# Kernel tuning notes

Hardware: AMD Instinct MI355X
Metric: run time of the kernel (lower is better)

Reference implementation:

```python
import jax, jax.numpy as jnp
import numpy as np

B = 1024      # batch
E = 1024      # encoding_dim
OUT = 34      # 17 joints x 2 coords


def setup_inputs() -> dict:
    key = jax.random.key(0)
    ks = jax.random.split(key, 8)
    s = 0.02  # weight init scale
    return {
        "h": jax.random.normal(ks[0], (B, E), dtype=jnp.float32),
        "c": jax.random.normal(ks[1], (B, E), dtype=jnp.float32),
        "W_ih": jax.random.normal(ks[2], (4 * E, E), dtype=jnp.float32) * s,
        "W_hh": jax.random.normal(ks[3], (4 * E, E), dtype=jnp.float32) * s,
        "b_ih": jax.random.normal(ks[4], (4 * E,), dtype=jnp.float32) * s,
        "b_hh": jax.random.normal(ks[5], (4 * E,), dtype=jnp.float32) * s,
        "W_out": jax.random.normal(ks[6], (OUT, E), dtype=jnp.float32) * s,
        "b_out": jax.random.normal(ks[7], (OUT,), dtype=jnp.float32) * s,
        "future_preds": 10,
    }


def reference(h, c, W_ih, W_hh, b_ih, b_hh, W_out, b_out, future_preds):
    E_ = h.shape[1]
    start = jnp.zeros_like(h)  # zeros=True start token

    def step(carry, _):
        h_t, c_t, x = carry
        # LSTMCell: gates in PyTorch order i, f, g, o
        gates = x @ W_ih.T + b_ih + h_t @ W_hh.T + b_hh  # [B, 4E]
        i = jax.nn.sigmoid(gates[:, 0 * E_:1 * E_])
        f = jax.nn.sigmoid(gates[:, 1 * E_:2 * E_])
        g = jnp.tanh(gates[:, 2 * E_:3 * E_])
        o = jax.nn.sigmoid(gates[:, 3 * E_:4 * E_])
        c_new = f * c_t + i * g
        h_new = o * jnp.tanh(c_new)
        return (h_new, c_new, h_new), h_new

    _, hs = jax.lax.scan(step, (h, c, start), None, length=future_preds)
    # hs: [T, B, E] -> [B, T, E]
    preds = jnp.transpose(hs, (1, 0, 2))
    return preds @ W_out.T + b_out  # [B, T, 34]
```

## Files before the change

kernel.cpp:

```cpp
#include <hip/hip_runtime.h>
#include <cstdint>
#include <cstddef>

#define E_DIM   1024
#define B_DIM   1024
#define T_STEPS 10
#define OUT_DIM 34
#define OUT_PAD 48
#define HSTR    24
#define QK      256
#define WQ_ELEMS (64 * QK)
#define DYN_LDS (2 * WQ_ELEMS * 2 + 128 * HSTR * 2)

typedef __attribute__((ext_vector_type(4))) float  f32x4;
typedef __attribute__((ext_vector_type(8))) __bf16 bf16x8;

__device__ __forceinline__ unsigned short f2bf(float f) {
    unsigned int u = __float_as_uint(f);
    u = (u + 0x7FFFu + ((u >> 16) & 1u)) >> 16;
    return (unsigned short)u;
}
__device__ __forceinline__ float sigmoid_(float x) { return 1.0f / (1.0f + __expf(-x)); }
__device__ __forceinline__ float tanh_(float x)    { return 2.0f / (1.0f + __expf(-2.0f * x)) - 1.0f; }

__global__ void prep_weights(const float* __restrict__ W_ih, const float* __restrict__ W_hh,
                             const float* __restrict__ b_ih, const float* __restrict__ b_hh,
                             unsigned short* __restrict__ Wsum, unsigned short* __restrict__ Whh,
                             float* __restrict__ bperm) {
    const int n = blockIdx.x;
    const int g = (n >> 4) & 3;
    const int e = ((n >> 6) << 4) | (n & 15);
    const int srow = g * E_DIM + e;
    const size_t src = (size_t)srow * E_DIM;
    const int k = threadIdx.x * 4;
    float4 wi = *(const float4*)(W_ih + src + k);
    float4 wh = *(const float4*)(W_hh + src + k);
    const size_t dst = (size_t)n * E_DIM + k;
    Wsum[dst + 0] = f2bf(wi.x + wh.x);
    Wsum[dst + 1] = f2bf(wi.y + wh.y);
    Wsum[dst + 2] = f2bf(wi.z + wh.z);
    Wsum[dst + 3] = f2bf(wi.w + wh.w);
    Whh[dst + 0] = f2bf(wh.x);
    Whh[dst + 1] = f2bf(wh.y);
    Whh[dst + 2] = f2bf(wh.z);
    Whh[dst + 3] = f2bf(wh.w);
    if (threadIdx.x == 0) bperm[n] = b_ih[srow] + b_hh[srow];
}

__global__ void prep_state(const float* __restrict__ h0, const float* __restrict__ W_out,
                           unsigned short* __restrict__ hbuf, unsigned short* __restrict__ Woutp) {
    const int b = blockIdx.x;
    const int t = threadIdx.x;
    if (b < 1024) {
        const size_t i = ((size_t)b * 256 + t) * 4;
        float4 hv = *(const float4*)(h0 + i);
        hbuf[i + 0] = f2bf(hv.x);
        hbuf[i + 1] = f2bf(hv.y);
        hbuf[i + 2] = f2bf(hv.z);
        hbuf[i + 3] = f2bf(hv.w);
    } else {
        const int o = b - 1024;
        const int k = t * 4;
        float4 w = make_float4(0.f, 0.f, 0.f, 0.f);
        if (o < OUT_DIM) w = *(const float4*)(W_out + (size_t)o * E_DIM + k);
        const size_t dst = (size_t)o * E_DIM + k;
        Woutp[dst + 0] = f2bf(w.x);
        Woutp[dst + 1] = f2bf(w.y);
        Woutp[dst + 2] = f2bf(w.z);
        Woutp[dst + 3] = f2bf(w.w);
    }
}

__global__ void prep_c(const float* __restrict__ c0, float* __restrict__ C) {
    const int m = blockIdx.x;
    const int e0 = threadIdx.x * 4;
    float4 v = *(const float4*)(c0 + (size_t)m * E_DIM + e0);
    const int bm = m >> 7, wave = (m >> 5) & 3, mt = (m >> 4) & 1, q = (m >> 2) & 3, r = m & 3;
    const float vv[4] = {v.x, v.y, v.z, v.w};
#pragma unroll
    for (int ii = 0; ii < 4; ++ii) {
        const int e = e0 + ii;
        const int bn = e >> 4, j = e & 15;
        const int lane = q * 16 + j;
        C[(((size_t)(bn * 8 + bm) * 4 + wave) * 64 + lane) * 8 + mt * 4 + r] = vv[ii];
    }
}

__global__ __launch_bounds__(256, 2) void lstm_step(
    const unsigned short* __restrict__ Wp,
    const float* __restrict__ bp,
    const unsigned short* __restrict__ Hin,
    float* __restrict__ C,
    unsigned short* __restrict__ Hout)
{
    extern __shared__ __align__(16) unsigned short smem[];
    unsigned short* Wbuf0 = smem;
    unsigned short* Wbuf1 = smem + WQ_ELEMS;
    unsigned short* Ht    = smem + 2 * WQ_ELEMS;

    const int tid  = threadIdx.x;
    const int wave = tid >> 6;
    const int lane = tid & 63;
    const int bn = blockIdx.x;
    const int bm = blockIdx.y;
    const int j  = lane & 15;
    const int q  = lane >> 4;
    const int j7 = j & 7;

    f32x4 acc[2][4];
#pragma unroll
    for (int a = 0; a < 2; ++a)
#pragma unroll
        for (int b = 0; b < 4; ++b) acc[a][b] = (f32x4){0.f, 0.f, 0.f, 0.f};

    const int nb = bn * 64 + j;
    const float bi = bp[nb +  0];
    const float bf = bp[nb + 16];
    const float bg = bp[nb + 32];
    const float bo = bp[nb + 48];
    const size_t cbase = (((size_t)(bn * 8 + bm) * 4 + wave) * 64 + lane) * 8;
    float4 cold0 = *(const float4*)(C + cbase);
    float4 cold1 = *(const float4*)(C + cbase + 4);

    const unsigned short* arow0 = Hin + (size_t)(bm * 128 + wave * 32 + j) * E_DIM + q * 8;
    const unsigned short* arow1 = arow0 + (size_t)16 * E_DIM;
    const unsigned short* wrow  = Wp + (size_t)(bn * 64) * E_DIM;

    uint4 ra[8][2];
#pragma unroll
    for (int p = 0; p < 8; ++p) {
        ra[p][0] = *(const uint4*)(arow0 + p * 32);
        ra[p][1] = *(const uint4*)(arow1 + p * 32);
    }

    uint4 wreg[8];
#pragma unroll
    for (int i = 0; i < 8; ++i) {
        const int s = i * 256 + tid, row = s >> 5, c = s & 31;
        wreg[i] = *(const uint4*)(wrow + (size_t)row * E_DIM + c * 8);
    }
#pragma unroll
    for (int i = 0; i < 8; ++i) {
        const int s = i * 256 + tid, row = s >> 5, c = s & 31;
        *(uint4*)(Wbuf0 + row * QK + ((c ^ (row & 7)) << 3)) = wreg[i];
    }
    __syncthreads();

    for (int qtr = 0; qtr < 4; ++qtr) {
        if (qtr < 3) {
#pragma unroll
            for (int i = 0; i < 8; ++i) {
                const int s = i * 256 + tid, row = s >> 5, c = s & 31;
                wreg[i] = *(const uint4*)(wrow + (size_t)row * E_DIM + (qtr + 1) * QK + c * 8);
            }
        }
        const unsigned short* wb = (qtr & 1) ? Wbuf1 : Wbuf0;
#pragma unroll
        for (int ks8 = 0; ks8 < 8; ++ks8) {
            const int ks = qtr * 8 + ks8;
            bf16x8 av0 = __builtin_bit_cast(bf16x8, ra[ks & 7][0]);
            bf16x8 av1 = __builtin_bit_cast(bf16x8, ra[ks & 7][1]);
            const int coff = ((ks8 * 4 + q) ^ j7) << 3;
            bf16x8 bv[4];
#pragma unroll
            for (int nt = 0; nt < 4; ++nt)
                bv[nt] = *(const bf16x8*)(wb + (nt * 16 + j) * QK + coff);
#pragma unroll
            for (int nt = 0; nt < 4; ++nt) {
                acc[0][nt] = __builtin_amdgcn_mfma_f32_16x16x32_bf16(av0, bv[nt], acc[0][nt], 0, 0, 0);
                acc[1][nt] = __builtin_amdgcn_mfma_f32_16x16x32_bf16(av1, bv[nt], acc[1][nt], 0, 0, 0);
            }
            if (ks < 24) {
                ra[ks & 7][0] = *(const uint4*)(arow0 + (ks + 8) * 32);
                ra[ks & 7][1] = *(const uint4*)(arow1 + (ks + 8) * 32);
            }
        }
        if (qtr < 3) {
            unsigned short* wn_ = ((qtr + 1) & 1) ? Wbuf1 : Wbuf0;
#pragma unroll
            for (int i = 0; i < 8; ++i) {
                const int s = i * 256 + tid, row = s >> 5, c = s & 31;
                *(uint4*)(wn_ + row * QK + ((c ^ (row & 7)) << 3)) = wreg[i];
            }
            __syncthreads();
        }
    }

    float4 cnew[2];
    const float coldv[2][4] = {{cold0.x, cold0.y, cold0.z, cold0.w},
                               {cold1.x, cold1.y, cold1.z, cold1.w}};
#pragma unroll
    for (int mt = 0; mt < 2; ++mt) {
#pragma unroll
        for (int r = 0; r < 4; ++r) {
            const float iv = sigmoid_(acc[mt][0][r] + bi);
            const float fv = sigmoid_(acc[mt][1][r] + bf);
            const float gv = tanh_(acc[mt][2][r] + bg);
            const float ov = sigmoid_(acc[mt][3][r] + bo);
            const float cn = fv * coldv[mt][r] + iv * gv;
            cnew[mt][r] = cn;
            const int rowl = wave * 32 + mt * 16 + q * 4 + r;
            Ht[rowl * HSTR + j] = f2bf(ov * tanh_(cn));
        }
    }
    *(float4*)(C + cbase)     = cnew[0];
    *(float4*)(C + cbase + 4) = cnew[1];
    __syncthreads();

    {
        const int row = tid >> 1, part = tid & 1;
        uint4 v = *(const uint4*)(Ht + row * HSTR + part * 8);
        *(uint4*)(Hout + (size_t)(bm * 128 + row) * E_DIM + bn * 16 + part * 8) = v;
    }
}

__global__ __launch_bounds__(256) void proj_kernel(
    const unsigned short* __restrict__ Hs,
    const unsigned short* __restrict__ Wo,
    const float* __restrict__ b_out,
    float* __restrict__ Out)
{
    __shared__ float red[4][32][OUT_PAD];

    const int tid = threadIdx.x, wave = tid >> 6, lane = tid & 63;
    const int j = lane & 15, q = lane >> 4;
    const int t  = blockIdx.y;
    const int bb = blockIdx.x;
    const unsigned short* Hbase = Hs + ((size_t)t * B_DIM + (size_t)bb * 32) * E_DIM;
    const int k0 = wave * 256;

    f32x4 acc[2][3];
#pragma unroll
    for (int a = 0; a < 2; ++a)
#pragma unroll
        for (int b = 0; b < 3; ++b) acc[a][b] = (f32x4){0.f, 0.f, 0.f, 0.f};

#pragma unroll
    for (int kk = 0; kk < 256; kk += 32) {
        const int kc = k0 + kk + q * 8;
        bf16x8 av[2], bv[3];
#pragma unroll
        for (int mt = 0; mt < 2; ++mt)
            av[mt] = *(const bf16x8*)(Hbase + (size_t)(mt * 16 + j) * E_DIM + kc);
#pragma unroll
        for (int nt = 0; nt < 3; ++nt)
            bv[nt] = *(const bf16x8*)(Wo + (size_t)(nt * 16 + j) * E_DIM + kc);
#pragma unroll
        for (int mt = 0; mt < 2; ++mt)
#pragma unroll
            for (int nt = 0; nt < 3; ++nt)
                acc[mt][nt] = __builtin_amdgcn_mfma_f32_16x16x32_bf16(av[mt], bv[nt], acc[mt][nt], 0, 0, 0);
    }

#pragma unroll
    for (int mt = 0; mt < 2; ++mt)
#pragma unroll
        for (int nt = 0; nt < 3; ++nt)
#pragma unroll
            for (int r = 0; r < 4; ++r)
                red[wave][mt * 16 + q * 4 + r][nt * 16 + j] = acc[mt][nt][r];
    __syncthreads();

#pragma unroll
    for (int ii = 0; ii < 6; ++ii) {
        const int idx = tid * 6 + ii;
        const int row = idx / OUT_PAD, o = idx % OUT_PAD;
        if (o < OUT_DIM) {
            const float s = red[0][row][o] + red[1][row][o] + red[2][row][o] + red[3][row][o];
            Out[((size_t)(bb * 32 + row) * T_STEPS + t) * OUT_DIM + o] = s + b_out[o];
        }
    }
}

extern "C" void kernel_launch(void* const* d_in, const int* in_sizes, int n_in,
                              void* d_out, int out_size, void* d_ws, size_t ws_size,
                              hipStream_t stream) {
    (void)in_sizes; (void)n_in; (void)out_size; (void)ws_size;
    const float* h     = (const float*)d_in[0];
    const float* c     = (const float*)d_in[1];
    const float* W_ih  = (const float*)d_in[2];
    const float* W_hh  = (const float*)d_in[3];
    const float* b_ih  = (const float*)d_in[4];
    const float* b_hh  = (const float*)d_in[5];
    const float* W_out = (const float*)d_in[6];
    const float* b_out = (const float*)d_in[7];
    float* out = (float*)d_out;

    char* ws = (char*)d_ws;
    unsigned short* Wsum  = (unsigned short*)(ws + 0);
    unsigned short* Whh   = (unsigned short*)(ws + 8388608);
    float*          bperm = (float*)(ws + 16777216);
    unsigned short* Woutp = (unsigned short*)(ws + 16842752);
    float*          cbuf  = (float*)(ws + 16941056);
    unsigned short* hs    = (unsigned short*)(ws + 21135360);

    hipFuncSetAttribute((const void*)lstm_step,
                        hipFuncAttributeMaxDynamicSharedMemorySize, DYN_LDS);

    prep_weights<<<4096, 256, 0, stream>>>(W_ih, W_hh, b_ih, b_hh, Wsum, Whh, bperm);
    prep_state<<<1072, 256, 0, stream>>>(h, W_out, hs, Woutp);
    prep_c<<<1024, 256, 0, stream>>>(c, cbuf);

    lstm_step<<<dim3(64, 8), 256, DYN_LDS, stream>>>(Whh, bperm, hs, cbuf,
                                                     hs + (size_t)B_DIM * E_DIM);
    for (int t = 1; t < T_STEPS; ++t)
        lstm_step<<<dim3(64, 8), 256, DYN_LDS, stream>>>(Wsum, bperm,
                                                         hs + (size_t)t * B_DIM * E_DIM,
                                                         cbuf,
                                                         hs + (size_t)(t + 1) * B_DIM * E_DIM);

    proj_kernel<<<dim3(32, T_STEPS), 256, 0, stream>>>(hs + (size_t)B_DIM * E_DIM,
                                                       Woutp, b_out, out);
}
```

Before: 333.3 us.

## Pre-arrange LSTM weights in MFMA fragment order for contiguous loads

The weight prep kernel now writes W_ih+W_hh and W_hh in bf16, pre-permuted into the exact per-lane MFMA B-fragment order for each block's tile and K quarter. The step kernel can then stream each quarter with fully contiguous global loads and read LDS at lane*8 strides, with no XOR swizzle or row/column index math. The bias permutation moves into prep_state, and prep_weights launches far fewer, larger blocks. In exchange the prep kernel issues scattered 2-byte stores, and the LDS read pattern loses the swizzle that was there to avoid bank conflicts.

```diff
diff --git a/kernel.cpp b/kernel.cpp
--- a/kernel.cpp
+++ b/kernel.cpp
@@ -23,32 +23,37 @@
 __device__ __forceinline__ float sigmoid_(float x) { return 1.0f / (1.0f + __expf(-x)); }
 __device__ __forceinline__ float tanh_(float x)    { return 2.0f / (1.0f + __expf(-2.0f * x)) - 1.0f; }
 
-__global__ void prep_weights(const float* __restrict__ W_ih, const float* __restrict__ W_hh,
-                             const float* __restrict__ b_ih, const float* __restrict__ b_hh,
-                             unsigned short* __restrict__ Wsum, unsigned short* __restrict__ Whh,
-                             float* __restrict__ bperm) {
-    const int n = blockIdx.x;
-    const int g = (n >> 4) & 3;
-    const int e = ((n >> 6) << 4) | (n & 15);
-    const int srow = g * E_DIM + e;
-    const size_t src = (size_t)srow * E_DIM;
-    const int k = threadIdx.x * 4;
-    float4 wi = *(const float4*)(W_ih + src + k);
-    float4 wh = *(const float4*)(W_hh + src + k);
-    const size_t dst = (size_t)n * E_DIM + k;
-    Wsum[dst + 0] = f2bf(wi.x + wh.x);
-    Wsum[dst + 1] = f2bf(wi.y + wh.y);
-    Wsum[dst + 2] = f2bf(wi.z + wh.z);
-    Wsum[dst + 3] = f2bf(wi.w + wh.w);
-    Whh[dst + 0] = f2bf(wh.x);
-    Whh[dst + 1] = f2bf(wh.y);
-    Whh[dst + 2] = f2bf(wh.z);
-    Whh[dst + 3] = f2bf(wh.w);
-    if (threadIdx.x == 0) bperm[n] = b_ih[srow] + b_hh[srow];
+__global__ void prep_weights_frag(const float* __restrict__ W_ih, const float* __restrict__ W_hh,
+                                  unsigned short* __restrict__ WsumF, unsigned short* __restrict__ WhhF) {
+    const int bn = blockIdx.x >> 2, qtr = blockIdx.x & 3;
+    const int nt = threadIdx.x >> 6, lane = threadIdx.x & 63;
+    const int j = lane & 15, q = lane >> 4;
+    const int srow = nt * E_DIM + bn * 16 + j;
+    const float* wi = W_ih + (size_t)srow * E_DIM;
+    const float* wh = W_hh + (size_t)srow * E_DIM;
+    const size_t dstb = (size_t)bn * 65536 + (size_t)qtr * 16384 + nt * 512 + lane * 8;
+#pragma unroll
+    for (int ks8 = 0; ks8 < 8; ++ks8) {
+        const int k = qtr * 256 + ks8 * 32 + q * 8;
+        float4 i0 = *(const float4*)(wi + k);
+        float4 i1 = *(const float4*)(wi + k + 4);
+        float4 h0 = *(const float4*)(wh + k);
+        float4 h1 = *(const float4*)(wh + k + 4);
+        unsigned short* ds = WsumF + dstb + ks8 * 2048;
+        unsigned short* dh = WhhF  + dstb + ks8 * 2048;
+        ds[0] = f2bf(i0.x + h0.x); ds[1] = f2bf(i0.y + h0.y);
+        ds[2] = f2bf(i0.z + h0.z); ds[3] = f2bf(i0.w + h0.w);
+        ds[4] = f2bf(i1.x + h1.x); ds[5] = f2bf(i1.y + h1.y);
+        ds[6] = f2bf(i1.z + h1.z); ds[7] = f2bf(i1.w + h1.w);
+        dh[0] = f2bf(h0.x); dh[1] = f2bf(h0.y); dh[2] = f2bf(h0.z); dh[3] = f2bf(h0.w);
+        dh[4] = f2bf(h1.x); dh[5] = f2bf(h1.y); dh[6] = f2bf(h1.z); dh[7] = f2bf(h1.w);
+    }
 }
 
 __global__ void prep_state(const float* __restrict__ h0, const float* __restrict__ W_out,
-                           unsigned short* __restrict__ hbuf, unsigned short* __restrict__ Woutp) {
+                           const float* __restrict__ b_ih, const float* __restrict__ b_hh,
+                           unsigned short* __restrict__ hbuf, unsigned short* __restrict__ Woutp,
+                           float* __restrict__ bperm) {
     const int b = blockIdx.x;
     const int t = threadIdx.x;
     if (b < 1024) {
@@ -58,7 +63,7 @@
         hbuf[i + 1] = f2bf(hv.y);
         hbuf[i + 2] = f2bf(hv.z);
         hbuf[i + 3] = f2bf(hv.w);
-    } else {
+    } else if (b < 1072) {
         const int o = b - 1024;
         const int k = t * 4;
         float4 w = make_float4(0.f, 0.f, 0.f, 0.f);
@@ -68,6 +73,12 @@
         Woutp[dst + 1] = f2bf(w.y);
         Woutp[dst + 2] = f2bf(w.z);
         Woutp[dst + 3] = f2bf(w.w);
+    } else {
+        const int n = (b - 1072) * 256 + t;
+        const int g = (n >> 4) & 3;
+        const int e = ((n >> 6) << 4) | (n & 15);
+        const int srow = g * E_DIM + e;
+        bperm[n] = b_ih[srow] + b_hh[srow];
     }
 }
 
@@ -87,7 +98,7 @@
 }
 
 __global__ __launch_bounds__(256, 2) void lstm_step(
-    const unsigned short* __restrict__ Wp,
+    const unsigned short* __restrict__ WF,
     const float* __restrict__ bp,
     const unsigned short* __restrict__ Hin,
     float* __restrict__ C,
@@ -105,7 +116,6 @@
     const int bm = blockIdx.y;
     const int j  = lane & 15;
     const int q  = lane >> 4;
-    const int j7 = j & 7;
 
     f32x4 acc[2][4];
 #pragma unroll
@@ -124,7 +134,7 @@
 
     const unsigned short* arow0 = Hin + (size_t)(bm * 128 + wave * 32 + j) * E_DIM + q * 8;
     const unsigned short* arow1 = arow0 + (size_t)16 * E_DIM;
-    const unsigned short* wrow  = Wp + (size_t)(bn * 64) * E_DIM;
+    const unsigned short* wsrc  = WF + (size_t)bn * 65536;
 
     uint4 ra[8][2];
 #pragma unroll
@@ -135,53 +145,44 @@
 
     uint4 wreg[8];
 #pragma unroll
-    for (int i = 0; i < 8; ++i) {
-        const int s = i * 256 + tid, row = s >> 5, c = s & 31;
-        wreg[i] = *(const uint4*)(wrow + (size_t)row * E_DIM + c * 8);
-    }
-#pragma unroll
-    for (int i = 0; i < 8; ++i) {
-        const int s = i * 256 + tid, row = s >> 5, c = s & 31;
-        *(uint4*)(Wbuf0 + row * QK + ((c ^ (row & 7)) << 3)) = wreg[i];
-    }
+    for (int i = 0; i < 8; ++i)
+        wreg[i] = *(const uint4*)(wsrc + (i * 256 + tid) * 8);
+#pragma unroll
+    for (int i = 0; i < 8; ++i)
+        *(uint4*)(Wbuf0 + (i * 256 + tid) * 8) = wreg[i];
     __syncthreads();
 
     for (int qtr = 0; qtr < 4; ++qtr) {
         if (qtr < 3) {
 #pragma unroll
-            for (int i = 0; i < 8; ++i) {
-                const int s = i * 256 + tid, row = s >> 5, c = s & 31;
-                wreg[i] = *(const uint4*)(wrow + (size_t)row * E_DIM + (qtr + 1) * QK + c * 8);
-            }
-        }
-        const unsigned short* wb = (qtr & 1) ? Wbuf1 : Wbuf0;
+            for (int i = 0; i < 8; ++i)
+                wreg[i] = *(const uint4*)(wsrc + (size_t)(qtr + 1) * WQ_ELEMS + (i * 256 + tid) * 8);
+        }
+        const unsigned short* wb = ((qtr & 1) ? Wbuf1 : Wbuf0) + lane * 8;
 #pragma unroll
         for (int ks8 = 0; ks8 < 8; ++ks8) {
             const int ks = qtr * 8 + ks8;
-            bf16x8 av0 = __builtin_bit_cast(bf16x8, ra[ks & 7][0]);
-            bf16x8 av1 = __builtin_bit_cast(bf16x8, ra[ks & 7][1]);
-            const int coff = ((ks8 * 4 + q) ^ j7) << 3;
+            bf16x8 av0 = __builtin_bit_cast(bf16x8, ra[ks8][0]);
+            bf16x8 av1 = __builtin_bit_cast(bf16x8, ra[ks8][1]);
             bf16x8 bv[4];
 #pragma unroll
             for (int nt = 0; nt < 4; ++nt)
-                bv[nt] = *(const bf16x8*)(wb + (nt * 16 + j) * QK + coff);
+                bv[nt] = *(const bf16x8*)(wb + (ks8 * 4 + nt) * 512);
 #pragma unroll
             for (int nt = 0; nt < 4; ++nt) {
                 acc[0][nt] = __builtin_amdgcn_mfma_f32_16x16x32_bf16(av0, bv[nt], acc[0][nt], 0, 0, 0);
                 acc[1][nt] = __builtin_amdgcn_mfma_f32_16x16x32_bf16(av1, bv[nt], acc[1][nt], 0, 0, 0);
             }
             if (ks < 24) {
-                ra[ks & 7][0] = *(const uint4*)(arow0 + (ks + 8) * 32);
-                ra[ks & 7][1] = *(const uint4*)(arow1 + (ks + 8) * 32);
+                ra[ks8][0] = *(const uint4*)(arow0 + (ks + 8) * 32);
+                ra[ks8][1] = *(const uint4*)(arow1 + (ks + 8) * 32);
             }
         }
         if (qtr < 3) {
             unsigned short* wn_ = ((qtr + 1) & 1) ? Wbuf1 : Wbuf0;
 #pragma unroll
-            for (int i = 0; i < 8; ++i) {
-                const int s = i * 256 + tid, row = s >> 5, c = s & 31;
-                *(uint4*)(wn_ + row * QK + ((c ^ (row & 7)) << 3)) = wreg[i];
-            }
+            for (int i = 0; i < 8; ++i)
+                *(uint4*)(wn_ + (i * 256 + tid) * 8) = wreg[i];
             __syncthreads();
         }
     }
@@ -287,8 +288,8 @@
     float* out = (float*)d_out;
 
     char* ws = (char*)d_ws;
-    unsigned short* Wsum  = (unsigned short*)(ws + 0);
-    unsigned short* Whh   = (unsigned short*)(ws + 8388608);
+    unsigned short* WsumF = (unsigned short*)(ws + 0);
+    unsigned short* WhhF  = (unsigned short*)(ws + 8388608);
     float*          bperm = (float*)(ws + 16777216);
     unsigned short* Woutp = (unsigned short*)(ws + 16842752);
     float*          cbuf  = (float*)(ws + 16941056);
@@ -297,14 +298,14 @@
     hipFuncSetAttribute((const void*)lstm_step,
                         hipFuncAttributeMaxDynamicSharedMemorySize, DYN_LDS);
 
-    prep_weights<<<4096, 256, 0, stream>>>(W_ih, W_hh, b_ih, b_hh, Wsum, Whh, bperm);
-    prep_state<<<1072, 256, 0, stream>>>(h, W_out, hs, Woutp);
+    prep_weights_frag<<<256, 256, 0, stream>>>(W_ih, W_hh, WsumF, WhhF);
+    prep_state<<<1088, 256, 0, stream>>>(h, W_out, b_ih, b_hh, hs, Woutp, bperm);
     prep_c<<<1024, 256, 0, stream>>>(c, cbuf);
 
-    lstm_step<<<dim3(64, 8), 256, DYN_LDS, stream>>>(Whh, bperm, hs, cbuf,
+    lstm_step<<<dim3(64, 8), 256, DYN_LDS, stream>>>(WhhF, bperm, hs, cbuf,
                                                      hs + (size_t)B_DIM * E_DIM);
     for (int t = 1; t < T_STEPS; ++t)
-        lstm_step<<<dim3(64, 8), 256, DYN_LDS, stream>>>(Wsum, bperm,
+        lstm_step<<<dim3(64, 8), 256, DYN_LDS, stream>>>(WsumF, bperm,
                                                          hs + (size_t)t * B_DIM * E_DIM,
                                                          cbuf,
                                                          hs + (size_t)(t + 1) * B_DIM * E_DIM);
```

New measurement: 329.5 us. Within noise of the previous version (-1.2%).
